# Performance work log

Hardware: AMD Instinct MI355X
Metric: run time of the kernel (lower is better)

## Reference

```python
import jax, jax.numpy as jnp
import numpy as np

N = 16384      # nodes
E = 262144     # edges (avg degree 16)
F_IN = 128     # n_feat
D = 128        # n_dims
C = 10         # n_clss
SIGMA = 1.0    # args.sigma


def setup_inputs() -> dict:
    key = jax.random.key(0)
    ks = jax.random.split(key, 12)
    s_in = 1.0 / np.sqrt(F_IN)
    s_d = 1.0 / np.sqrt(D)
    s_c = 1.0 / np.sqrt(2 * D)
    return {
        "x": jax.random.normal(ks[0], (N, F_IN), jnp.float32),
        "edge_index": jax.random.randint(ks[1], (2, E), 0, N, dtype=jnp.int32),
        # SAGEConv1: lin_l (neighbors, with bias) and lin_r (root, no bias)
        "W1l": jax.random.normal(ks[2], (D, F_IN), jnp.float32) * s_in,
        "b1l": jnp.zeros((D,), jnp.float32),
        "W1r": jax.random.normal(ks[3], (D, F_IN), jnp.float32) * s_in,
        # SAGEConv2
        "W2l": jax.random.normal(ks[4], (D, D), jnp.float32) * s_d,
        "b2l": jnp.zeros((D,), jnp.float32),
        "W2r": jax.random.normal(ks[5], (D, D), jnp.float32) * s_d,
        # anchor vector (init.uniform_ -> U[0,1))
        "aux": jax.random.uniform(ks[6], (D,), jnp.float32),
        # classifier on [h, z] concat
        "Wc": jax.random.normal(ks[7], (C, 2 * D), jnp.float32) * s_c,
        "bc": jnp.zeros((C,), jnp.float32),
    }


def _sage_conv(x, src, dst, Wl, bl, Wr):
    # PyG SAGEConv (mean aggr): out = lin_l(mean_{j in N(i)} x_j) + lin_r(x_i)
    msg = x[src]                                                  # [E, d]
    agg = jax.ops.segment_sum(msg, dst, num_segments=N)           # [N, d]
    deg = jax.ops.segment_sum(jnp.ones((src.shape[0],), x.dtype), dst,
                              num_segments=N)                     # [N]
    agg = agg / jnp.maximum(deg, 1.0)[:, None]
    return agg @ Wl.T + bl + x @ Wr.T


def _kernel_aggregate(h, aux, sigma):
    # cosine similarity to anchor (torch eps = 1e-8)
    eps = 1e-8
    hn = jnp.maximum(jnp.linalg.norm(h, axis=-1), eps)            # [N]
    an = jnp.maximum(jnp.linalg.norm(aux), eps)
    score = (h @ aux) / (hn * an)                                 # [N]
    diff = score[None, :] - score[:, None]                        # [N, N]
    kappa = jnp.exp(-(diff * diff) / (sigma * sigma))             # [N, N]
    return (kappa @ h) / jnp.sum(kappa, axis=1, keepdims=True)    # [N, d]


def reference(x, W1l, b1l, W1r, W2l, b2l, W2r, aux, Wc, bc, edge_index):
    src, dst = edge_index[0], edge_index[1]
    h = jax.nn.relu(_sage_conv(x, src, dst, W1l, b1l, W1r))
    # dropout is identity at inference
    h = _sage_conv(h, src, dst, W2l, b2l, W2r)
    z = _kernel_aggregate(h, aux, SIGMA)
    return jnp.concatenate([h, z], axis=-1) @ Wc.T + bc           # [N, C]
```

## Files before the change

### kernel.cpp

```cpp
#include <hip/hip_runtime.h>
#include <hip/hip_bf16.h>

#define D 128
#define KTERMS 16

typedef __attribute__((ext_vector_type(8))) short bf16x8;
typedef __attribute__((ext_vector_type(4))) float f32x4;

__device__ inline short rne_bf16(float f) {
    union { float f; unsigned u; } v; v.f = f;
    unsigned r = (v.u + 0x7fffu + ((v.u >> 16) & 1u)) >> 16;
    return (short)r;
}
__device__ inline float bf16_to_f(unsigned s) {
    union { unsigned u; float f; } v; v.u = s << 16;
    return v.f;
}
__device__ inline unsigned pk2(float a, float b) {
    return (unsigned)(unsigned short)rne_bf16(a) | ((unsigned)(unsigned short)rne_bf16(b) << 16);
}

__global__ __launch_bounds__(256) void prep_kernel(const float* __restrict__ x,
                                                   short* __restrict__ xb,
                                                   const float* __restrict__ W1l,
                                                   const float* __restrict__ W1r,
                                                   const float* __restrict__ W2l,
                                                   const float* __restrict__ W2r,
                                                   short* __restrict__ Bc1,
                                                   short* __restrict__ Bc2) {
    int b = blockIdx.x;
    if (b < 1024) {
        int base = (b * 256 + threadIdx.x) * 8;
        const float4 a = *reinterpret_cast<const float4*>(&x[base]);
        const float4 c = *reinterpret_cast<const float4*>(&x[base + 4]);
        uint4 o;
        o.x = pk2(a.x, a.y);
        o.y = pk2(a.z, a.w);
        o.z = pk2(c.x, c.y);
        o.w = pk2(c.z, c.w);
        *reinterpret_cast<uint4*>(&xb[base]) = o;
    } else {
        int idx = (b - 1024) * 256 + threadIdx.x;
        int layer = idx >> 15;
        int rem = idx & 32767;
        int c = rem >> 8, k = rem & 255;
        const float* Wl = layer ? W2l : W1l;
        const float* Wr = layer ? W2r : W1r;
        float v = (k < 128) ? Wl[c * 128 + k] : Wr[c * 128 + (k - 128)];
        short* Bc = layer ? Bc2 : Bc1;
        Bc[c * 256 + k] = rne_bf16(v);
    }
}

__global__ __launch_bounds__(256) void degi_kernel(const int* __restrict__ dst,
                                                   int* __restrict__ degi, int E) {
    int e = blockIdx.x * 256 + threadIdx.x;
    if (e < E) atomicAdd(&degi[dst[e]], 1);
}

__global__ __launch_bounds__(1024) void scan_kernel(const int* __restrict__ degi,
                                                    int* __restrict__ rowptr,
                                                    float* __restrict__ invdeg, int N) {
    __shared__ int part[1024];
    int tid = threadIdx.x;
    int base = tid * 16;
    int loc[16];
    int s = 0;
#pragma unroll
    for (int i = 0; i < 16; i++) {
        int d = degi[base + i];
        loc[i] = s; s += d;
        invdeg[base + i] = 1.0f / fmaxf((float)d, 1.0f);
    }
    part[tid] = s;
    __syncthreads();
    for (int off = 1; off < 1024; off <<= 1) {
        int t = (tid >= off) ? part[tid - off] : 0;
        __syncthreads();
        if (tid >= off) part[tid] += t;
        __syncthreads();
    }
    int prefix = part[tid] - s;
#pragma unroll
    for (int i = 0; i < 16; i++) rowptr[base + i] = prefix + loc[i];
    if (tid == 1023) rowptr[N] = prefix + s;
}

__global__ __launch_bounds__(256) void fill_kernel(const int* __restrict__ src,
                                                   const int* __restrict__ dst,
                                                   const int* __restrict__ rowptr,
                                                   int* __restrict__ cursor,
                                                   int* __restrict__ csr_src, int E) {
    int e = blockIdx.x * 256 + threadIdx.x;
    if (e < E) {
        int d = dst[e];
        int pos = atomicAdd(&cursor[d], 1);
        csr_src[rowptr[d] + pos] = src[e];
    }
}

__global__ __launch_bounds__(256) void gatherb_kernel(const short* __restrict__ xin,
                                                      const int* __restrict__ rowptr,
                                                      const int* __restrict__ csr_src,
                                                      const float* __restrict__ invdeg,
                                                      short* __restrict__ aggb, int N) {
    int lane = threadIdx.x & 63;
    int wid = threadIdx.x >> 6;
    int sub = lane >> 4;
    int sl = lane & 15;
    int node = (blockIdx.x * 4 + wid) * 4 + sub;
    if (node >= N) return;
    int beg = rowptr[node], end = rowptr[node + 1];
    float acc[8] = {0.0f, 0.0f, 0.0f, 0.0f, 0.0f, 0.0f, 0.0f, 0.0f};
    for (int j = beg; j < end; j++) {
        int s = csr_src[j];
        const uint4 v = *reinterpret_cast<const uint4*>(&xin[(size_t)s * D + sl * 8]);
        acc[0] += bf16_to_f(v.x & 0xffffu);
        acc[1] += bf16_to_f(v.x >> 16);
        acc[2] += bf16_to_f(v.y & 0xffffu);
        acc[3] += bf16_to_f(v.y >> 16);
        acc[4] += bf16_to_f(v.z & 0xffffu);
        acc[5] += bf16_to_f(v.z >> 16);
        acc[6] += bf16_to_f(v.w & 0xffffu);
        acc[7] += bf16_to_f(v.w >> 16);
    }
    float inv = invdeg[node];
    uint4 o;
    o.x = pk2(acc[0] * inv, acc[1] * inv);
    o.y = pk2(acc[2] * inv, acc[3] * inv);
    o.z = pk2(acc[4] * inv, acc[5] * inv);
    o.w = pk2(acc[6] * inv, acc[7] * inv);
    *reinterpret_cast<uint4*>(&aggb[(size_t)node * D + sl * 8]) = o;
}

__global__ __launch_bounds__(256) void sage_mfma_kernel(const short* __restrict__ Aagg,
                                                        const short* __restrict__ Aroot,
                                                        const short* __restrict__ Bc,
                                                        const float* __restrict__ bias,
                                                        const float* __restrict__ aux,
                                                        short* __restrict__ outb,
                                                        float* __restrict__ outf,
                                                        float* __restrict__ sbuf,
                                                        float* __restrict__ wbuf,
                                                        int relu, int score) {
    __shared__ float sdot[32][2];
    __shared__ float snrm[32][2];
    __shared__ float an_s;

    int lane = threadIdx.x & 63;
    int wid = threadIdx.x >> 6;
    int row0 = blockIdx.x * 32;

    if (score && wid == 0) {
        float2 av = *reinterpret_cast<const float2*>(&aux[lane * 2]);
        float na = av.x * av.x + av.y * av.y;
        for (int m = 1; m < 64; m <<= 1) na += __shfl_xor(na, m);
        if (lane == 0) an_s = fmaxf(sqrtf(na), 1e-8f);
    }

    int arow = row0 + (wid & 1) * 16 + (lane & 15);
    int colq = lane & 15;
    int koff = (lane >> 4) * 8;
    int colbase = (wid >> 1) * 64;

    f32x4 acc[4];
#pragma unroll
    for (int t = 0; t < 4; t++) acc[t] = (f32x4){0.0f, 0.0f, 0.0f, 0.0f};

#pragma unroll
    for (int kc = 0; kc < 8; kc++) {
        const short* Asrc = (kc < 4) ? Aagg : Aroot;
        int k = (kc & 3) * 32 + koff;
        bf16x8 a = *reinterpret_cast<const bf16x8*>(&Asrc[(size_t)arow * D + k]);
#pragma unroll
        for (int t = 0; t < 4; t++) {
            int col = colbase + t * 16 + colq;
            bf16x8 b = *reinterpret_cast<const bf16x8*>(&Bc[(size_t)col * 256 + kc * 32 + koff]);
            acc[t] = __builtin_amdgcn_mfma_f32_16x16x32_bf16(a, b, acc[t], 0, 0, 0);
        }
    }

    int rbase_l = (wid & 1) * 16 + (lane >> 4) * 4;
    float dotp[4] = {0.0f, 0.0f, 0.0f, 0.0f};
    float nrmp[4] = {0.0f, 0.0f, 0.0f, 0.0f};
#pragma unroll
    for (int t = 0; t < 4; t++) {
        int col = colbase + t * 16 + colq;
        float bv = bias[col];
        float av = score ? aux[col] : 0.0f;
#pragma unroll
        for (int r = 0; r < 4; r++) {
            float v = acc[t][r] + bv;
            if (relu) v = fmaxf(v, 0.0f);
            if (outf) outf[(size_t)(row0 + rbase_l + r) * D + col] = v;
            else outb[(size_t)(row0 + rbase_l + r) * D + col] = rne_bf16(v);
            dotp[r] += v * av;
            nrmp[r] += v * v;
        }
    }

    if (score) {
#pragma unroll
        for (int m = 1; m < 16; m <<= 1) {
#pragma unroll
            for (int r = 0; r < 4; r++) {
                dotp[r] += __shfl_xor(dotp[r], m);
                nrmp[r] += __shfl_xor(nrmp[r], m);
            }
        }
        if ((lane & 15) == 0) {
#pragma unroll
            for (int r = 0; r < 4; r++) {
                sdot[rbase_l + r][wid >> 1] = dotp[r];
                snrm[rbase_l + r][wid >> 1] = nrmp[r];
            }
        }
        __syncthreads();
        int tid = threadIdx.x;
        if (tid < 32) {
            float dot = sdot[tid][0] + sdot[tid][1];
            float nh = snrm[tid][0] + snrm[tid][1];
            float hn = fmaxf(sqrtf(nh), 1e-8f);
            float sc = dot / (hn * an_s);
            sbuf[row0 + tid] = sc;
            wbuf[row0 + tid] = expf(-sc * sc);
        }
    }
}

__global__ __launch_bounds__(512) void moments_kernel(const float* __restrict__ h,
                                                      const float* __restrict__ sbuf,
                                                      const float* __restrict__ wbuf,
                                                      float* __restrict__ M,
                                                      float* __restrict__ mden, int N) {
    __shared__ float lds[8 * KTERMS * D];
    __shared__ float ldsm[8 * KTERMS];
    int tid = threadIdx.x;
    int w = tid >> 6, lane = tid & 63;
    int j0 = blockIdx.x * 64 + w * 8;

    float2 acc[KTERMS];
    float macc[KTERMS];
#pragma unroll
    for (int k = 0; k < KTERMS; k++) { acc[k] = make_float2(0.0f, 0.0f); macc[k] = 0.0f; }

    for (int j = j0; j < j0 + 8; j++) {
        float sj = sbuf[j];
        float wj = wbuf[j];
        float2 hv = *reinterpret_cast<const float2*>(&h[(size_t)j * D + lane * 2]);
        float coef = wj;
#pragma unroll
        for (int k = 0; k < KTERMS; k++) {
            acc[k].x += coef * hv.x;
            acc[k].y += coef * hv.y;
            macc[k] += coef;
            coef *= sj;
        }
    }

#pragma unroll
    for (int k = 0; k < KTERMS; k++) {
        lds[(w * KTERMS + k) * D + lane * 2]     = acc[k].x;
        lds[(w * KTERMS + k) * D + lane * 2 + 1] = acc[k].y;
    }
    if (lane == 0) {
#pragma unroll
        for (int k = 0; k < KTERMS; k++) ldsm[w * KTERMS + k] = macc[k];
    }
    __syncthreads();

    for (int e = tid; e < KTERMS * D; e += 512) {
        float s = 0.0f;
#pragma unroll
        for (int ww = 0; ww < 8; ww++) s += lds[ww * KTERMS * D + e];
        atomicAdd(&M[e], s);
    }
    if (tid < KTERMS) {
        float s = 0.0f;
#pragma unroll
        for (int ww = 0; ww < 8; ww++) s += ldsm[ww * KTERMS + tid];
        atomicAdd(&mden[tid], s);
    }
}

__global__ __launch_bounds__(128) void zcls_kernel(const float* __restrict__ M,
                                                   const float* __restrict__ mden,
                                                   const float* __restrict__ sbuf,
                                                   const float* __restrict__ h,
                                                   const float* __restrict__ Wc,
                                                   const float* __restrict__ bc,
                                                   float* __restrict__ out, int N) {
    const float A[KTERMS] = {1.0f, 2.0f, 2.0f, 1.3333334f, 0.6666667f, 0.26666668f,
                             0.08888889f, 0.025396826f, 0.0063492064f, 0.0014109347f,
                             2.8218695e-4f, 5.1306718e-5f, 8.5511196e-6f, 1.3155569e-6f,
                             1.8793670e-7f, 2.5058226e-8f};
    __shared__ float Ml[KTERMS * D];
    __shared__ float ml[KTERMS];
    __shared__ float wls[10 * 256];
    __shared__ float red[10][2];
    int tid = threadIdx.x;
    int lane = tid & 63, w = tid >> 6;
#pragma unroll
    for (int k = 0; k < KTERMS; k++) Ml[k * D + tid] = M[k * D + tid];
    if (tid < KTERMS) ml[tid] = mden[tid];
    for (int e = tid; e < 10 * 256; e += 128) wls[e] = Wc[e];
    __syncthreads();

    int n0 = blockIdx.x * 16;
    for (int n = n0; n < n0 + 16; n++) {
        float si = sbuf[n];
        float num = 0.0f, den = 0.0f, p = 1.0f;
#pragma unroll
        for (int k = 0; k < KTERMS; k++) {
            float ck = A[k] * p;
            num += ck * Ml[k * D + tid];
            den += ck * ml[k];
            p *= si;
        }
        float zc = num / den;
        float hc = h[(size_t)n * D + tid];

        float part[10];
#pragma unroll
        for (int c = 0; c < 10; c++)
            part[c] = hc * wls[c * 256 + tid] + zc * wls[c * 256 + 128 + tid];
#pragma unroll
        for (int m = 1; m < 64; m <<= 1) {
#pragma unroll
            for (int c = 0; c < 10; c++) part[c] += __shfl_xor(part[c], m);
        }
        if (lane == 0) {
#pragma unroll
            for (int c = 0; c < 10; c++) red[c][w] = part[c];
        }
        __syncthreads();
        if (tid < 10) out[(size_t)n * 10 + tid] = red[tid][0] + red[tid][1] + bc[tid];
        __syncthreads();
    }
}

extern "C" void kernel_launch(void* const* d_in, const int* in_sizes, int n_in,
                              void* d_out, int out_size, void* d_ws, size_t ws_size,
                              hipStream_t stream) {
    const float* x   = (const float*)d_in[0];
    const int*   ei  = (const int*)d_in[1];
    const float* W1l = (const float*)d_in[2];
    const float* b1l = (const float*)d_in[3];
    const float* W1r = (const float*)d_in[4];
    const float* W2l = (const float*)d_in[5];
    const float* b2l = (const float*)d_in[6];
    const float* W2r = (const float*)d_in[7];
    const float* aux = (const float*)d_in[8];
    const float* Wc  = (const float*)d_in[9];
    const float* bc  = (const float*)d_in[10];
    float* out = (float*)d_out;

    const int N = in_sizes[0] / D;
    const int E = in_sizes[1] / 2;
    const int* srcArr = ei;
    const int* dstArr = ei + E;
    const size_t ND = (size_t)N * D;

    int* ip = (int*)d_ws;
    int* degi    = ip; ip += N;
    int* cursor  = ip; ip += N;
    int* rowptr  = ip; ip += N + 1;
    int* csr_src = ip; ip += E;
    uintptr_t up = ((uintptr_t)ip + 15) & ~(uintptr_t)15;
    short* sp = (short*)up;
    short* xb   = sp; sp += ND;
    short* aggb = sp; sp += ND;
    short* h1b  = sp; sp += ND;
    short* Bc1  = sp; sp += 128 * 256;
    short* Bc2  = sp; sp += 128 * 256;
    up = ((uintptr_t)sp + 15) & ~(uintptr_t)15;
    float* p = (float*)up;
    float* invdeg = p; p += N;
    float* sbuf   = p; p += N;
    float* wbuf   = p; p += N;
    float* M      = p; p += KTERMS * D;
    float* mden   = p; p += KTERMS;
    float* h2     = p; p += ND;

    hipMemsetAsync(degi, 0, (size_t)(2 * N) * sizeof(int), stream);
    hipMemsetAsync(M, 0, (size_t)(KTERMS * D + KTERMS) * sizeof(float), stream);

    prep_kernel<<<1280, 256, 0, stream>>>(x, xb, W1l, W1r, W2l, W2r, Bc1, Bc2);

    degi_kernel<<<(E + 255) / 256, 256, 0, stream>>>(dstArr, degi, E);
    scan_kernel<<<1, 1024, 0, stream>>>(degi, rowptr, invdeg, N);
    fill_kernel<<<(E + 255) / 256, 256, 0, stream>>>(srcArr, dstArr, rowptr, cursor, csr_src, E);

    gatherb_kernel<<<N / 16, 256, 0, stream>>>(xb, rowptr, csr_src, invdeg, aggb, N);
    sage_mfma_kernel<<<N / 32, 256, 0, stream>>>(aggb, xb, Bc1, b1l, aux,
                                                 h1b, nullptr, nullptr, nullptr, 1, 0);
    gatherb_kernel<<<N / 16, 256, 0, stream>>>(h1b, rowptr, csr_src, invdeg, aggb, N);
    sage_mfma_kernel<<<N / 32, 256, 0, stream>>>(aggb, h1b, Bc2, b2l, aux,
                                                 nullptr, h2, sbuf, wbuf, 0, 1);

    moments_kernel<<<N / 64, 512, 0, stream>>>(h2, sbuf, wbuf, M, mden, N);

    zcls_kernel<<<N / 16, 128, 0, stream>>>(M, mden, sbuf, h2, Wc, bc, out, N);
}
```

Baseline: 160.3 us.

## Fuse neighbor gather into SAGE MFMA kernel and fold memsets into prep

```diff
diff --git a/kernel.cpp b/kernel.cpp
--- a/kernel.cpp
+++ b/kernel.cpp
@@ -18,6 +18,16 @@
 }
 __device__ inline unsigned pk2(float a, float b) {
     return (unsigned)(unsigned short)rne_bf16(a) | ((unsigned)(unsigned short)rne_bf16(b) << 16);
+}
+__device__ inline void addv(float* acc, uint4 v) {
+    acc[0] += bf16_to_f(v.x & 0xffffu);
+    acc[1] += bf16_to_f(v.x >> 16);
+    acc[2] += bf16_to_f(v.y & 0xffffu);
+    acc[3] += bf16_to_f(v.y >> 16);
+    acc[4] += bf16_to_f(v.z & 0xffffu);
+    acc[5] += bf16_to_f(v.z >> 16);
+    acc[6] += bf16_to_f(v.w & 0xffffu);
+    acc[7] += bf16_to_f(v.w >> 16);
 }
 
 __global__ __launch_bounds__(256) void prep_kernel(const float* __restrict__ x,
@@ -27,10 +37,13 @@
                                                    const float* __restrict__ W2l,
                                                    const float* __restrict__ W2r,
                                                    short* __restrict__ Bc1,
-                                                   short* __restrict__ Bc2) {
+                                                   short* __restrict__ Bc2,
+                                                   int* __restrict__ zero_ints,
+                                                   float* __restrict__ zero_f) {
     int b = blockIdx.x;
+    int tid = threadIdx.x;
     if (b < 1024) {
-        int base = (b * 256 + threadIdx.x) * 8;
+        int base = (b * 256 + tid) * 8;
         const float4 a = *reinterpret_cast<const float4*>(&x[base]);
         const float4 c = *reinterpret_cast<const float4*>(&x[base + 4]);
         uint4 o;
@@ -39,8 +52,8 @@
         o.z = pk2(c.x, c.y);
         o.w = pk2(c.z, c.w);
         *reinterpret_cast<uint4*>(&xb[base]) = o;
-    } else {
-        int idx = (b - 1024) * 256 + threadIdx.x;
+    } else if (b < 1280) {
+        int idx = (b - 1024) * 256 + tid;
         int layer = idx >> 15;
         int rem = idx & 32767;
         int c = rem >> 8, k = rem & 255;
@@ -49,6 +62,11 @@
         float v = (k < 128) ? Wl[c * 128 + k] : Wr[c * 128 + (k - 128)];
         short* Bc = layer ? Bc2 : Bc1;
         Bc[c * 256 + k] = rne_bf16(v);
+    } else if (b < 1312) {
+        int idx = (b - 1280) * 256 + tid;
+        reinterpret_cast<int4*>(zero_ints)[idx] = make_int4(0, 0, 0, 0);
+    } else {
+        for (int e = tid; e < KTERMS * D + KTERMS; e += 256) zero_f[e] = 0.0f;
     }
 }
 
@@ -99,57 +117,27 @@
     }
 }
 
-__global__ __launch_bounds__(256) void gatherb_kernel(const short* __restrict__ xin,
-                                                      const int* __restrict__ rowptr,
-                                                      const int* __restrict__ csr_src,
-                                                      const float* __restrict__ invdeg,
-                                                      short* __restrict__ aggb, int N) {
+__global__ __launch_bounds__(256) void sage_fused_kernel(const short* __restrict__ Asrc,
+                                                         const short* __restrict__ Bc,
+                                                         const float* __restrict__ bias,
+                                                         const int* __restrict__ rowptr,
+                                                         const int* __restrict__ csr_src,
+                                                         const float* __restrict__ invdeg,
+                                                         const float* __restrict__ aux,
+                                                         short* __restrict__ outb,
+                                                         float* __restrict__ outf,
+                                                         float* __restrict__ sbuf,
+                                                         float* __restrict__ wbuf,
+                                                         int relu, int score) {
+    __shared__ short aggl[16 * 128];
+    __shared__ float sdot[16][4];
+    __shared__ float snrm[16][4];
+    __shared__ float an_s;
+
     int lane = threadIdx.x & 63;
     int wid = threadIdx.x >> 6;
-    int sub = lane >> 4;
-    int sl = lane & 15;
-    int node = (blockIdx.x * 4 + wid) * 4 + sub;
-    if (node >= N) return;
-    int beg = rowptr[node], end = rowptr[node + 1];
-    float acc[8] = {0.0f, 0.0f, 0.0f, 0.0f, 0.0f, 0.0f, 0.0f, 0.0f};
-    for (int j = beg; j < end; j++) {
-        int s = csr_src[j];
-        const uint4 v = *reinterpret_cast<const uint4*>(&xin[(size_t)s * D + sl * 8]);
-        acc[0] += bf16_to_f(v.x & 0xffffu);
-        acc[1] += bf16_to_f(v.x >> 16);
-        acc[2] += bf16_to_f(v.y & 0xffffu);
-        acc[3] += bf16_to_f(v.y >> 16);
-        acc[4] += bf16_to_f(v.z & 0xffffu);
-        acc[5] += bf16_to_f(v.z >> 16);
-        acc[6] += bf16_to_f(v.w & 0xffffu);
-        acc[7] += bf16_to_f(v.w >> 16);
-    }
-    float inv = invdeg[node];
-    uint4 o;
-    o.x = pk2(acc[0] * inv, acc[1] * inv);
-    o.y = pk2(acc[2] * inv, acc[3] * inv);
-    o.z = pk2(acc[4] * inv, acc[5] * inv);
-    o.w = pk2(acc[6] * inv, acc[7] * inv);
-    *reinterpret_cast<uint4*>(&aggb[(size_t)node * D + sl * 8]) = o;
-}
-
-__global__ __launch_bounds__(256) void sage_mfma_kernel(const short* __restrict__ Aagg,
-                                                        const short* __restrict__ Aroot,
-                                                        const short* __restrict__ Bc,
-                                                        const float* __restrict__ bias,
-                                                        const float* __restrict__ aux,
-                                                        short* __restrict__ outb,
-                                                        float* __restrict__ outf,
-                                                        float* __restrict__ sbuf,
-                                                        float* __restrict__ wbuf,
-                                                        int relu, int score) {
-    __shared__ float sdot[32][2];
-    __shared__ float snrm[32][2];
-    __shared__ float an_s;
-
-    int lane = threadIdx.x & 63;
-    int wid = threadIdx.x >> 6;
-    int row0 = blockIdx.x * 32;
+    int row0 = blockIdx.x * 16;
+    int sub = lane >> 4, sl = lane & 15;
 
     if (score && wid == 0) {
         float2 av = *reinterpret_cast<const float2*>(&aux[lane * 2]);
@@ -158,44 +146,79 @@
         if (lane == 0) an_s = fmaxf(sqrtf(na), 1e-8f);
     }
 
-    int arow = row0 + (wid & 1) * 16 + (lane & 15);
-    int colq = lane & 15;
-    int koff = (lane >> 4) * 8;
-    int colbase = (wid >> 1) * 64;
-
-    f32x4 acc[4];
-#pragma unroll
-    for (int t = 0; t < 4; t++) acc[t] = (f32x4){0.0f, 0.0f, 0.0f, 0.0f};
+    int r = wid * 4 + sub;
+    int node = row0 + r;
+    int beg = rowptr[node], end = rowptr[node + 1];
+    float acc8[8] = {0.0f, 0.0f, 0.0f, 0.0f, 0.0f, 0.0f, 0.0f, 0.0f};
+    int j = beg;
+    for (; j + 3 < end; j += 4) {
+        int s0 = csr_src[j], s1 = csr_src[j + 1], s2 = csr_src[j + 2], s3 = csr_src[j + 3];
+        uint4 v0 = *reinterpret_cast<const uint4*>(&Asrc[(size_t)s0 * D + sl * 8]);
+        uint4 v1 = *reinterpret_cast<const uint4*>(&Asrc[(size_t)s1 * D + sl * 8]);
+        uint4 v2 = *reinterpret_cast<const uint4*>(&Asrc[(size_t)s2 * D + sl * 8]);
+        uint4 v3 = *reinterpret_cast<const uint4*>(&Asrc[(size_t)s3 * D + sl * 8]);
+        addv(acc8, v0); addv(acc8, v1); addv(acc8, v2); addv(acc8, v3);
+    }
+    for (; j < end; j++) {
+        int s = csr_src[j];
+        uint4 v = *reinterpret_cast<const uint4*>(&Asrc[(size_t)s * D + sl * 8]);
+        addv(acc8, v);
+    }
+    float inv = invdeg[node];
+    uint4 o;
+    o.x = pk2(acc8[0] * inv, acc8[1] * inv);
+    o.y = pk2(acc8[2] * inv, acc8[3] * inv);
+    o.z = pk2(acc8[4] * inv, acc8[5] * inv);
+    o.w = pk2(acc8[6] * inv, acc8[7] * inv);
+    int wbyte = (r * 256 + sl * 16) ^ ((r & 7) << 4);
+    *reinterpret_cast<uint4*>(reinterpret_cast<char*>(aggl) + wbyte) = o;
+    __syncthreads();
+
+    int colbase = wid * 32;
+    int rl = lane & 15;
+    int kg = lane >> 4;
+    int koff = kg * 8;
+    int arow_g = row0 + rl;
+
+    f32x4 acc[2];
+    acc[0] = (f32x4){0.0f, 0.0f, 0.0f, 0.0f};
+    acc[1] = (f32x4){0.0f, 0.0f, 0.0f, 0.0f};
 
 #pragma unroll
     for (int kc = 0; kc < 8; kc++) {
-        const short* Asrc = (kc < 4) ? Aagg : Aroot;
-        int k = (kc & 3) * 32 + koff;
-        bf16x8 a = *reinterpret_cast<const bf16x8*>(&Asrc[(size_t)arow * D + k]);
-#pragma unroll
-        for (int t = 0; t < 4; t++) {
-            int col = colbase + t * 16 + colq;
+        bf16x8 a;
+        if (kc < 4) {
+            int rbyte = (rl * 256 + kc * 64 + kg * 16) ^ ((rl & 7) << 4);
+            a = *reinterpret_cast<const bf16x8*>(reinterpret_cast<const char*>(aggl) + rbyte);
+        } else {
+            int k = (kc - 4) * 32 + koff;
+            a = *reinterpret_cast<const bf16x8*>(&Asrc[(size_t)arow_g * D + k]);
+        }
+#pragma unroll
+        for (int t = 0; t < 2; t++) {
+            int col = colbase + t * 16 + rl;
             bf16x8 b = *reinterpret_cast<const bf16x8*>(&Bc[(size_t)col * 256 + kc * 32 + koff]);
             acc[t] = __builtin_amdgcn_mfma_f32_16x16x32_bf16(a, b, acc[t], 0, 0, 0);
         }
     }
 
-    int rbase_l = (wid & 1) * 16 + (lane >> 4) * 4;
+    int rbase = kg * 4;
     float dotp[4] = {0.0f, 0.0f, 0.0f, 0.0f};
     float nrmp[4] = {0.0f, 0.0f, 0.0f, 0.0f};
 #pragma unroll
-    for (int t = 0; t < 4; t++) {
-        int col = colbase + t * 16 + colq;
+    for (int t = 0; t < 2; t++) {
+        int col = colbase + t * 16 + rl;
         float bv = bias[col];
         float av = score ? aux[col] : 0.0f;
 #pragma unroll
-        for (int r = 0; r < 4; r++) {
-            float v = acc[t][r] + bv;
+        for (int rr = 0; rr < 4; rr++) {
+            float v = acc[t][rr] + bv;
             if (relu) v = fmaxf(v, 0.0f);
-            if (outf) outf[(size_t)(row0 + rbase_l + r) * D + col] = v;
-            else outb[(size_t)(row0 + rbase_l + r) * D + col] = rne_bf16(v);
-            dotp[r] += v * av;
-            nrmp[r] += v * v;
+            int grow = row0 + rbase + rr;
+            if (outf) outf[(size_t)grow * D + col] = v;
+            else outb[(size_t)grow * D + col] = rne_bf16(v);
+            dotp[rr] += v * av;
+            nrmp[rr] += v * v;
         }
     }
 
@@ -203,23 +226,23 @@
 #pragma unroll
         for (int m = 1; m < 16; m <<= 1) {
 #pragma unroll
-            for (int r = 0; r < 4; r++) {
-                dotp[r] += __shfl_xor(dotp[r], m);
-                nrmp[r] += __shfl_xor(nrmp[r], m);
+            for (int rr = 0; rr < 4; rr++) {
+                dotp[rr] += __shfl_xor(dotp[rr], m);
+                nrmp[rr] += __shfl_xor(nrmp[rr], m);
             }
         }
-        if ((lane & 15) == 0) {
-#pragma unroll
-            for (int r = 0; r < 4; r++) {
-                sdot[rbase_l + r][wid >> 1] = dotp[r];
-                snrm[rbase_l + r][wid >> 1] = nrmp[r];
+        if (rl == 0) {
+#pragma unroll
+            for (int rr = 0; rr < 4; rr++) {
+                sdot[rbase + rr][wid] = dotp[rr];
+                snrm[rbase + rr][wid] = nrmp[rr];
             }
         }
         __syncthreads();
         int tid = threadIdx.x;
-        if (tid < 32) {
-            float dot = sdot[tid][0] + sdot[tid][1];
-            float nh = snrm[tid][0] + snrm[tid][1];
+        if (tid < 16) {
+            float dot = sdot[tid][0] + sdot[tid][1] + sdot[tid][2] + sdot[tid][3];
+            float nh  = snrm[tid][0] + snrm[tid][1] + snrm[tid][2] + snrm[tid][3];
             float hn = fmaxf(sqrtf(nh), 1e-8f);
             float sc = dot / (hn * an_s);
             sbuf[row0 + tid] = sc;
@@ -369,7 +392,6 @@
     uintptr_t up = ((uintptr_t)ip + 15) & ~(uintptr_t)15;
     short* sp = (short*)up;
     short* xb   = sp; sp += ND;
-    short* aggb = sp; sp += ND;
     short* h1b  = sp; sp += ND;
     short* Bc1  = sp; sp += 128 * 256;
     short* Bc2  = sp; sp += 128 * 256;
@@ -382,21 +404,16 @@
     float* mden   = p; p += KTERMS;
     float* h2     = p; p += ND;
 
-    hipMemsetAsync(degi, 0, (size_t)(2 * N) * sizeof(int), stream);
-    hipMemsetAsync(M, 0, (size_t)(KTERMS * D + KTERMS) * sizeof(float), stream);
-
-    prep_kernel<<<1280, 256, 0, stream>>>(x, xb, W1l, W1r, W2l, W2r, Bc1, Bc2);
+    prep_kernel<<<1313, 256, 0, stream>>>(x, xb, W1l, W1r, W2l, W2r, Bc1, Bc2, degi, M);
 
     degi_kernel<<<(E + 255) / 256, 256, 0, stream>>>(dstArr, degi, E);
     scan_kernel<<<1, 1024, 0, stream>>>(degi, rowptr, invdeg, N);
     fill_kernel<<<(E + 255) / 256, 256, 0, stream>>>(srcArr, dstArr, rowptr, cursor, csr_src, E);
 
-    gatherb_kernel<<<N / 16, 256, 0, stream>>>(xb, rowptr, csr_src, invdeg, aggb, N);
-    sage_mfma_kernel<<<N / 32, 256, 0, stream>>>(aggb, xb, Bc1, b1l, aux,
-                                                 h1b, nullptr, nullptr, nullptr, 1, 0);
-    gatherb_kernel<<<N / 16, 256, 0, stream>>>(h1b, rowptr, csr_src, invdeg, aggb, N);
-    sage_mfma_kernel<<<N / 32, 256, 0, stream>>>(aggb, h1b, Bc2, b2l, aux,
-                                                 nullptr, h2, sbuf, wbuf, 0, 1);
+    sage_fused_kernel<<<N / 16, 256, 0, stream>>>(xb, Bc1, b1l, rowptr, csr_src, invdeg,
+                                                  aux, h1b, nullptr, nullptr, nullptr, 1, 0);
+    sage_fused_kernel<<<N / 16, 256, 0, stream>>>(h1b, Bc2, b2l, rowptr, csr_src, invdeg,
+                                                  aux, nullptr, h2, sbuf, wbuf, 0, 1);
 
     moments_kernel<<<N / 64, 512, 0, stream>>>(h2, sbuf, wbuf, M, mden, N);
 
```

Measured after the change: 134.1 us. 16.3% less time.
